# Performance work log

Measured on AMD Instinct MI355X. Metric: run time of the kernel, lower is better.

Reference implementation:

```python
import jax, jax.numpy as jnp
import numpy as np

T = 4096
EMBED = 1024
HEADS = 16


def setup_inputs() -> dict:
    key = jax.random.key(0)
    kx, kq, kk, kv = jax.random.split(key, 4)
    bound = 1.0 / np.sqrt(EMBED)
    x = jax.random.normal(kx, (T, EMBED), dtype=jnp.float32)
    Wq = jax.random.uniform(kq, (EMBED, EMBED), minval=-bound, maxval=bound, dtype=jnp.float32)
    Wk = jax.random.uniform(kk, (EMBED, EMBED), minval=-bound, maxval=bound, dtype=jnp.float32)
    Wv = jax.random.uniform(kv, (EMBED, EMBED), minval=-bound, maxval=bound, dtype=jnp.float32)
    return {"x": x, "Wq": Wq, "Wk": Wk, "Wv": Wv}


def reference(x, Wq, Wk, Wv):
    t, e = x.shape
    h = HEADS
    c = e // h  # head dim
    q = (x @ Wq).reshape(t, h, c)
    k = (x @ Wk).reshape(t, h, c)
    v = (x @ Wv).reshape(t, h, c)
    # scores: [h, t, t]
    scores = jnp.einsum('qhc,khc->hqk', q, k) / jnp.sqrt(jnp.asarray(c, x.dtype))
    causal = jnp.tril(jnp.ones((t, t), dtype=bool))
    scores = jnp.where(causal[None, :, :], scores, -jnp.inf)  # same as + log(tril)
    p = jax.nn.softmax(scores, axis=-1)
    y = jnp.einsum('hqk,khc->qhc', p, v)  # [t, h, c]
    return y.reshape(t, e)
```

## Files before the change

### kernel.cpp

```cpp
#include <hip/hip_runtime.h>
#include <hip/hip_bf16.h>

#define T_SEQ 4096
#define EMB 1024
#define NH 16
#define HD 64
#define QBLK 128
#define KVB 64
#define DEFER_THR 10.0f

typedef float f32x4 __attribute__((ext_vector_type(4)));
typedef float f32x16 __attribute__((ext_vector_type(16)));
typedef short short8 __attribute__((ext_vector_type(8)));
typedef short short4v __attribute__((ext_vector_type(4)));

__device__ inline unsigned short f2bf(float f) {
  union { float f; unsigned u; } a; a.f = f;
  unsigned r = a.u + 0x7fffu + ((a.u >> 16) & 1u);
  return (unsigned short)(r >> 16);
}
#if __has_builtin(__builtin_amdgcn_exp2f)
#define EXP2F(x) __builtin_amdgcn_exp2f(x)
#else
#define EXP2F(x) exp2f(x)
#endif
#define GLL16(g, l) __builtin_amdgcn_global_load_lds( \
    (const __attribute__((address_space(1))) void*)(g), \
    (__attribute__((address_space(3))) void*)(l), 16, 0, 0)

__global__ __launch_bounds__(256) void cast_x_kernel(const float* __restrict__ in,
                                                     unsigned short* __restrict__ out) {
  int i = (blockIdx.x * 256 + threadIdx.x) * 8;
  float4 a = *(const float4*)(in + i);
  float4 b = *(const float4*)(in + i + 4);
  uint4 o;
  o.x = f2bf(a.x) | ((unsigned)f2bf(a.y) << 16);
  o.y = f2bf(a.z) | ((unsigned)f2bf(a.w) << 16);
  o.z = f2bf(b.x) | ((unsigned)f2bf(b.y) << 16);
  o.w = f2bf(b.z) | ((unsigned)f2bf(b.w) << 16);
  *(uint4*)(out + i) = o;
}

__global__ __launch_bounds__(256) void transpose_cast_kernel(const float* __restrict__ Wq,
                                                             const float* __restrict__ Wk,
                                                             const float* __restrict__ Wv,
                                                             unsigned short* __restrict__ WTall) {
  int z = blockIdx.z;
  const float* W = (z == 0) ? Wq : ((z == 1) ? Wk : Wv);
  unsigned short* WT = WTall + (size_t)z * EMB * EMB;
  __shared__ unsigned short tile[32][33];
  int tx = threadIdx.x & 31, ty = threadIdx.x >> 5;
  int bn = blockIdx.x * 32, bk = blockIdx.y * 32;
#pragma unroll
  for (int p = 0; p < 4; p++)
    tile[ty + p * 8][tx] = f2bf(W[(size_t)(bk + ty + p * 8) * EMB + bn + tx]);
  __syncthreads();
#pragma unroll
  for (int p = 0; p < 4; p++)
    WT[(size_t)(bn + ty + p * 8) * EMB + bk + tx] = tile[tx][ty + p * 8];
}

__global__ __launch_bounds__(256) void gemm_qkv(const unsigned short* __restrict__ Xb,
                                                const unsigned short* __restrict__ WTall,
                                                unsigned short* __restrict__ QKV) {
  int z = blockIdx.z;
  const unsigned short* Bt = WTall + (size_t)z * EMB * EMB;
  unsigned short* Out = QKV + (size_t)z * T_SEQ * EMB;

  __shared__ __align__(16) unsigned short sA[128 * 32];
  __shared__ __align__(16) unsigned short sB[128 * 32];

  int m0 = blockIdx.x * 128, n0 = blockIdx.y * 128;
  int tid = threadIdx.x;
  int lane = tid & 63, wid = tid >> 6;
  int wr = wid >> 1, wc = wid & 1;
  int fr = lane & 15, fq = lane >> 4;

  int r0 = tid >> 2, o0 = (tid & 3) * 8;
  int r1 = (tid + 256) >> 2;

  f32x4 acc[4][4] = {};

  for (int k0 = 0; k0 < EMB; k0 += 32) {
    __syncthreads();
    GLL16(Xb + (size_t)(m0 + r0) * EMB + k0 + o0, sA + (size_t)tid * 8);
    GLL16(Xb + (size_t)(m0 + r1) * EMB + k0 + o0, sA + (size_t)(tid + 256) * 8);
    GLL16(Bt + (size_t)(n0 + r0) * EMB + k0 + o0, sB + (size_t)tid * 8);
    GLL16(Bt + (size_t)(n0 + r1) * EMB + k0 + o0, sB + (size_t)(tid + 256) * 8);
    asm volatile("s_waitcnt vmcnt(0)" ::: "memory");
    __syncthreads();

    short8 aF[4], bF[4];
#pragma unroll
    for (int i = 0; i < 4; i++) {
      aF[i] = *(const short8*)(sA + (wr * 64 + i * 16 + fr) * 32 + fq * 8);
      bF[i] = *(const short8*)(sB + (wc * 64 + i * 16 + fr) * 32 + fq * 8);
    }
#pragma unroll
    for (int i = 0; i < 4; i++)
#pragma unroll
      for (int j = 0; j < 4; j++)
        acc[i][j] = __builtin_amdgcn_mfma_f32_16x16x32_bf16(aF[i], bF[j], acc[i][j], 0, 0, 0);
  }

  if (z == 2) {
#pragma unroll
    for (int i = 0; i < 4; i++)
#pragma unroll
      for (int j = 0; j < 4; j++) {
        int col = n0 + wc * 64 + j * 16 + fr;
        int row0 = m0 + wr * 64 + i * 16 + fq * 4;
        short4v pk4;
#pragma unroll
        for (int r = 0; r < 4; r++) pk4[r] = (short)f2bf(acc[i][j][r]);
        *(short4v*)(Out + (size_t)col * T_SEQ + row0) = pk4;
      }
  } else {
    float scale = (z == 0) ? 0.1803368801111204f : 1.0f;
#pragma unroll
    for (int i = 0; i < 4; i++)
#pragma unroll
      for (int j = 0; j < 4; j++)
#pragma unroll
        for (int r = 0; r < 4; r++) {
          int row = m0 + wr * 64 + i * 16 + fq * 4 + r;
          int col = n0 + wc * 64 + j * 16 + fr;
          Out[(size_t)row * EMB + col] = f2bf(acc[i][j][r] * scale);
        }
  }
}

__global__ __launch_bounds__(256) void attn_kernel(const unsigned short* __restrict__ Qb,
                                                   const unsigned short* __restrict__ Kb,
                                                   const unsigned short* __restrict__ VTg,
                                                   float* __restrict__ out) {
  int qb = (gridDim.x - 1) - blockIdx.x;
  int h = blockIdx.y;
  int q0 = qb * QBLK;
  int tid = threadIdx.x;
  int lane = tid & 63, w = tid >> 6;
  int ql = lane & 31, hi = lane >> 5;

  __shared__ __align__(16) unsigned short smem[14336];
  unsigned short* sK = smem;
  unsigned short* sVT = smem + 64 * 72;
  unsigned short* sP = smem + 2 * 64 * 72 + w * (32 * 40);

  int wq0 = q0 + w * 32;
  int qg = wq0 + ql;

  short8 qf[4];
#pragma unroll
  for (int ks = 0; ks < 4; ks++)
    qf[ks] = *(const short8*)(Qb + (size_t)qg * EMB + h * HD + ks * 16 + hi * 8);

  f32x16 oT0 = {}, oT1 = {};
  float m = -1e30f, lsum = 0.f;

  int sr = tid >> 3;
  int scs = (tid & 7) * 8;

  int wqmax = wq0 + 31;
  int ntiles = (q0 + QBLK) / KVB;

  short8 ka = *(const short8*)(Kb + (size_t)(sr) * EMB + h * HD + scs);
  short8 kb = *(const short8*)(Kb + (size_t)(sr + 32) * EMB + h * HD + scs);
  short8 va = *(const short8*)(VTg + (size_t)(h * HD + sr) * T_SEQ + scs);
  short8 vb = *(const short8*)(VTg + (size_t)(h * HD + sr + 32) * T_SEQ + scs);

  for (int t = 0; t < ntiles; t++) {
    int kv0 = t * KVB;
    __syncthreads();
    *(short8*)(sK + sr * 72 + scs) = ka;
    *(short8*)(sK + (sr + 32) * 72 + scs) = kb;
    *(short8*)(sVT + sr * 72 + scs) = va;
    *(short8*)(sVT + (sr + 32) * 72 + scs) = vb;
    __syncthreads();

    if (t + 1 < ntiles) {
      int kv1 = kv0 + KVB;
      ka = *(const short8*)(Kb + (size_t)(kv1 + sr) * EMB + h * HD + scs);
      kb = *(const short8*)(Kb + (size_t)(kv1 + sr + 32) * EMB + h * HD + scs);
      va = *(const short8*)(VTg + (size_t)(h * HD + sr) * T_SEQ + kv1 + scs);
      vb = *(const short8*)(VTg + (size_t)(h * HD + sr + 32) * T_SEQ + kv1 + scs);
    }

#pragma unroll
    for (int s = 0; s < 2; s++) {
      int kvs = kv0 + s * 32;
      if (kvs <= wqmax) {
        f32x16 st = {};
        __builtin_amdgcn_s_setprio(1);
#pragma unroll
        for (int ks = 0; ks < 4; ks++) {
          short8 kf = *(const short8*)(sK + (s * 32 + ql) * 72 + ks * 16 + hi * 8);
          st = __builtin_amdgcn_mfma_f32_32x32x16_bf16(kf, qf[ks], st, 0, 0, 0);
        }
        __builtin_amdgcn_s_setprio(0);
        if (kvs + 31 > wq0) {
#pragma unroll
          for (int r = 0; r < 16; r++) {
            int kvg = kvs + (r & 3) + 8 * (r >> 2) + 4 * hi;
            if (kvg > qg) st[r] = -1e30f;
          }
        }
        float a0 = fmaxf(fmaxf(st[0], st[1]), st[2]);
        float a1 = fmaxf(fmaxf(st[3], st[4]), st[5]);
        float a2 = fmaxf(fmaxf(st[6], st[7]), st[8]);
        float a3 = fmaxf(fmaxf(st[9], st[10]), st[11]);
        float a4 = fmaxf(fmaxf(st[12], st[13]), st[14]);
        float mt = fmaxf(fmaxf(fmaxf(a0, a1), a2), fmaxf(fmaxf(a3, a4), st[15]));
        mt = fmaxf(mt, __shfl_xor(mt, 32));
        if (!__all(mt - m <= DEFER_THR)) {
          float mnew = fmaxf(m, mt);
          float al = EXP2F(m - mnew);
          lsum *= al;
#pragma unroll
          for (int r = 0; r < 16; r++) { oT0[r] *= al; oT1[r] *= al; }
          m = mnew;
        }
#pragma unroll
        for (int r = 0; r < 16; r++) st[r] = EXP2F(st[r] - m);
        float s0 = (st[0] + st[1]) + (st[2] + st[3]);
        float s1 = (st[4] + st[5]) + (st[6] + st[7]);
        float s2 = (st[8] + st[9]) + (st[10] + st[11]);
        float s3 = (st[12] + st[13]) + (st[14] + st[15]);
        float ls = (s0 + s1) + (s2 + s3);
        ls += __shfl_xor(ls, 32);
        lsum += ls;

#pragma unroll
        for (int g = 0; g < 4; g++) {
          __hip_bfloat162 plo = __float22bfloat162_rn(float2{st[g * 4 + 0], st[g * 4 + 1]});
          __hip_bfloat162 phi = __float22bfloat162_rn(float2{st[g * 4 + 2], st[g * 4 + 3]});
          union { __hip_bfloat162 h[2]; short4v s4; } u4;
          u4.h[0] = plo; u4.h[1] = phi;
          *(short4v*)(sP + ql * 40 + g * 8 + hi * 4) = u4.s4;
        }
        asm volatile("s_waitcnt lgkmcnt(0)" ::: "memory");
        __builtin_amdgcn_sched_barrier(0);

        __builtin_amdgcn_s_setprio(1);
#pragma unroll
        for (int ksp = 0; ksp < 2; ksp++) {
          short8 pa = *(const short8*)(sP + ql * 40 + ksp * 16 + hi * 8);
          int cb = s * 32 + ksp * 16 + hi * 8;
          short8 v0 = *(const short8*)(sVT + (0 * 32 + ql) * 72 + cb);
          short8 v1 = *(const short8*)(sVT + (1 * 32 + ql) * 72 + cb);
          oT0 = __builtin_amdgcn_mfma_f32_32x32x16_bf16(v0, pa, oT0, 0, 0, 0);
          oT1 = __builtin_amdgcn_mfma_f32_32x32x16_bf16(v1, pa, oT1, 0, 0, 0);
        }
        __builtin_amdgcn_s_setprio(0);
      }
    }
  }

  float inv = 1.0f / lsum;
  float* sw = (float*)smem + w * (32 * 36);
  int orow = lane >> 1, ocol = (lane & 1) * 16;
#pragma unroll
  for (int dt = 0; dt < 2; dt++) {
    __syncthreads();
#pragma unroll
    for (int r = 0; r < 16; r++) {
      int dl = (r & 3) + 8 * (r >> 2) + 4 * hi;
      sw[ql * 36 + dl] = (dt ? oT1[r] : oT0[r]) * inv;
    }
    __syncthreads();
#pragma unroll
    for (int c = 0; c < 4; c++) {
      f32x4 vv = *(const f32x4*)(sw + orow * 36 + ocol + c * 4);
      *(f32x4*)(out + (size_t)(wq0 + orow) * EMB + h * HD + dt * 32 + ocol + c * 4) = vv;
    }
  }
}

extern "C" void kernel_launch(void* const* d_in, const int* in_sizes, int n_in,
                              void* d_out, int out_size, void* d_ws, size_t ws_size,
                              hipStream_t stream) {
  const float* x  = (const float*)d_in[0];
  const float* Wq = (const float*)d_in[1];
  const float* Wk = (const float*)d_in[2];
  const float* Wv = (const float*)d_in[3];
  float* out = (float*)d_out;

  unsigned short* Qb = (unsigned short*)d_ws;
  unsigned short* Kb = Qb + (size_t)T_SEQ * EMB;
  unsigned short* VT = Kb + (size_t)T_SEQ * EMB;
  unsigned short* Xb = VT + (size_t)T_SEQ * EMB;
  unsigned short* WT = Xb + (size_t)T_SEQ * EMB;

  cast_x_kernel<<<(T_SEQ * EMB) / (256 * 8), 256, 0, stream>>>(x, Xb);
  dim3 tg(EMB / 32, EMB / 32, 3);
  transpose_cast_kernel<<<tg, 256, 0, stream>>>(Wq, Wk, Wv, WT);
  dim3 gg(T_SEQ / 128, EMB / 128, 3);
  gemm_qkv<<<gg, 256, 0, stream>>>(Xb, WT, Qb);
  dim3 ag(T_SEQ / QBLK, NH);
  attn_kernel<<<ag, 256, 0, stream>>>(Qb, Kb, VT, out);
}
```

Before: 251.0 us.

## Split KV range across waves per 32-query block with LDS merge of softmax partials

Attention now gives each block one 32-row query tile and spreads the causal KV sub-tiles round-robin across its four waves. K and V fragments are loaded straight from global memory into registers with no shared-memory staging or block barriers in the loop. Per-wave max and sum partials are then merged through LDS in a final reduction. V is written row-major by the GEMM and transposed by a separate new kernel, which adds a launch and extra traffic, and the launch-bounds hint now asks for more resident blocks.

```diff
diff --git a/kernel.cpp b/kernel.cpp
--- a/kernel.cpp
+++ b/kernel.cpp
@@ -5,8 +5,6 @@
 #define EMB 1024
 #define NH 16
 #define HD 64
-#define QBLK 128
-#define KVB 64
 #define DEFER_THR 10.0f
 
 typedef float f32x4 __attribute__((ext_vector_type(4)));
@@ -60,6 +58,21 @@
     WT[(size_t)(bn + ty + p * 8) * EMB + bk + tx] = tile[tx][ty + p * 8];
 }
 
+__global__ __launch_bounds__(256) void transpose_v_kernel(const unsigned short* __restrict__ V,
+                                                          unsigned short* __restrict__ VT) {
+  int h = blockIdx.z;
+  int t0 = blockIdx.x * 32, d0 = blockIdx.y * 32;
+  __shared__ unsigned short tl[32][33];
+  int tx = threadIdx.x & 31, ty = threadIdx.x >> 5;
+#pragma unroll
+  for (int p = 0; p < 4; p++)
+    tl[ty + p * 8][tx] = V[(size_t)(t0 + ty + p * 8) * EMB + h * HD + d0 + tx];
+  __syncthreads();
+#pragma unroll
+  for (int p = 0; p < 4; p++)
+    VT[(size_t)(h * HD + d0 + ty + p * 8) * T_SEQ + t0 + tx] = tl[tx][ty + p * 8];
+}
+
 __global__ __launch_bounds__(256) void gemm_qkv(const unsigned short* __restrict__ Xb,
                                                 const unsigned short* __restrict__ WTall,
                                                 unsigned short* __restrict__ QKV) {
@@ -103,51 +116,36 @@
         acc[i][j] = __builtin_amdgcn_mfma_f32_16x16x32_bf16(aF[i], bF[j], acc[i][j], 0, 0, 0);
   }
 
-  if (z == 2) {
-#pragma unroll
-    for (int i = 0; i < 4; i++)
-#pragma unroll
-      for (int j = 0; j < 4; j++) {
+  float scale = (z == 0) ? 0.1803368801111204f : 1.0f;
+#pragma unroll
+  for (int i = 0; i < 4; i++)
+#pragma unroll
+    for (int j = 0; j < 4; j++)
+#pragma unroll
+      for (int r = 0; r < 4; r++) {
+        int row = m0 + wr * 64 + i * 16 + fq * 4 + r;
         int col = n0 + wc * 64 + j * 16 + fr;
-        int row0 = m0 + wr * 64 + i * 16 + fq * 4;
-        short4v pk4;
-#pragma unroll
-        for (int r = 0; r < 4; r++) pk4[r] = (short)f2bf(acc[i][j][r]);
-        *(short4v*)(Out + (size_t)col * T_SEQ + row0) = pk4;
+        Out[(size_t)row * EMB + col] = f2bf(acc[i][j][r] * scale);
       }
-  } else {
-    float scale = (z == 0) ? 0.1803368801111204f : 1.0f;
-#pragma unroll
-    for (int i = 0; i < 4; i++)
-#pragma unroll
-      for (int j = 0; j < 4; j++)
-#pragma unroll
-        for (int r = 0; r < 4; r++) {
-          int row = m0 + wr * 64 + i * 16 + fq * 4 + r;
-          int col = n0 + wc * 64 + j * 16 + fr;
-          Out[(size_t)row * EMB + col] = f2bf(acc[i][j][r] * scale);
-        }
-  }
-}
-
-__global__ __launch_bounds__(256) void attn_kernel(const unsigned short* __restrict__ Qb,
-                                                   const unsigned short* __restrict__ Kb,
-                                                   const unsigned short* __restrict__ VTg,
-                                                   float* __restrict__ out) {
-  int qb = (gridDim.x - 1) - blockIdx.x;
+}
+
+__global__ __launch_bounds__(256, 4) void attn_kernel(const unsigned short* __restrict__ Qb,
+                                                      const unsigned short* __restrict__ Kb,
+                                                      const unsigned short* __restrict__ VTg,
+                                                      float* __restrict__ out) {
+  int c = (gridDim.x - 1) - blockIdx.x;
   int h = blockIdx.y;
-  int q0 = qb * QBLK;
   int tid = threadIdx.x;
   int lane = tid & 63, w = tid >> 6;
   int ql = lane & 31, hi = lane >> 5;
-
-  __shared__ __align__(16) unsigned short smem[14336];
-  unsigned short* sK = smem;
-  unsigned short* sVT = smem + 64 * 72;
-  unsigned short* sP = smem + 2 * 64 * 72 + w * (32 * 40);
-
-  int wq0 = q0 + w * 32;
-  int qg = wq0 + ql;
+  int wq0 = c * 32, qg = wq0 + ql;
+
+  __shared__ __align__(16) float smemf[4608];
+  unsigned short* sP = (unsigned short*)smemf + w * 1280;
+  float* bufA = smemf;
+  float* bufB = smemf + 2176;
+  float* sM = smemf + 4352;
+  float* sL = smemf + 4480;
 
   short8 qf[4];
 #pragma unroll
@@ -157,122 +155,117 @@
   f32x16 oT0 = {}, oT1 = {};
   float m = -1e30f, lsum = 0.f;
 
-  int sr = tid >> 3;
-  int scs = (tid & 7) * 8;
-
-  int wqmax = wq0 + 31;
-  int ntiles = (q0 + QBLK) / KVB;
-
-  short8 ka = *(const short8*)(Kb + (size_t)(sr) * EMB + h * HD + scs);
-  short8 kb = *(const short8*)(Kb + (size_t)(sr + 32) * EMB + h * HD + scs);
-  short8 va = *(const short8*)(VTg + (size_t)(h * HD + sr) * T_SEQ + scs);
-  short8 vb = *(const short8*)(VTg + (size_t)(h * HD + sr + 32) * T_SEQ + scs);
-
-  for (int t = 0; t < ntiles; t++) {
-    int kv0 = t * KVB;
-    __syncthreads();
-    *(short8*)(sK + sr * 72 + scs) = ka;
-    *(short8*)(sK + (sr + 32) * 72 + scs) = kb;
-    *(short8*)(sVT + sr * 72 + scs) = va;
-    *(short8*)(sVT + (sr + 32) * 72 + scs) = vb;
-    __syncthreads();
-
-    if (t + 1 < ntiles) {
-      int kv1 = kv0 + KVB;
-      ka = *(const short8*)(Kb + (size_t)(kv1 + sr) * EMB + h * HD + scs);
-      kb = *(const short8*)(Kb + (size_t)(kv1 + sr + 32) * EMB + h * HD + scs);
-      va = *(const short8*)(VTg + (size_t)(h * HD + sr) * T_SEQ + kv1 + scs);
-      vb = *(const short8*)(VTg + (size_t)(h * HD + sr + 32) * T_SEQ + kv1 + scs);
-    }
-
-#pragma unroll
-    for (int s = 0; s < 2; s++) {
-      int kvs = kv0 + s * 32;
-      if (kvs <= wqmax) {
-        f32x16 st = {};
-        __builtin_amdgcn_s_setprio(1);
-#pragma unroll
-        for (int ks = 0; ks < 4; ks++) {
-          short8 kf = *(const short8*)(sK + (s * 32 + ql) * 72 + ks * 16 + hi * 8);
-          st = __builtin_amdgcn_mfma_f32_32x32x16_bf16(kf, qf[ks], st, 0, 0, 0);
-        }
-        __builtin_amdgcn_s_setprio(0);
-        if (kvs + 31 > wq0) {
-#pragma unroll
-          for (int r = 0; r < 16; r++) {
-            int kvg = kvs + (r & 3) + 8 * (r >> 2) + 4 * hi;
-            if (kvg > qg) st[r] = -1e30f;
-          }
-        }
-        float a0 = fmaxf(fmaxf(st[0], st[1]), st[2]);
-        float a1 = fmaxf(fmaxf(st[3], st[4]), st[5]);
-        float a2 = fmaxf(fmaxf(st[6], st[7]), st[8]);
-        float a3 = fmaxf(fmaxf(st[9], st[10]), st[11]);
-        float a4 = fmaxf(fmaxf(st[12], st[13]), st[14]);
-        float mt = fmaxf(fmaxf(fmaxf(a0, a1), a2), fmaxf(fmaxf(a3, a4), st[15]));
-        mt = fmaxf(mt, __shfl_xor(mt, 32));
-        if (!__all(mt - m <= DEFER_THR)) {
-          float mnew = fmaxf(m, mt);
-          float al = EXP2F(m - mnew);
-          lsum *= al;
-#pragma unroll
-          for (int r = 0; r < 16; r++) { oT0[r] *= al; oT1[r] *= al; }
-          m = mnew;
-        }
-#pragma unroll
-        for (int r = 0; r < 16; r++) st[r] = EXP2F(st[r] - m);
-        float s0 = (st[0] + st[1]) + (st[2] + st[3]);
-        float s1 = (st[4] + st[5]) + (st[6] + st[7]);
-        float s2 = (st[8] + st[9]) + (st[10] + st[11]);
-        float s3 = (st[12] + st[13]) + (st[14] + st[15]);
-        float ls = (s0 + s1) + (s2 + s3);
-        ls += __shfl_xor(ls, 32);
-        lsum += ls;
-
-#pragma unroll
-        for (int g = 0; g < 4; g++) {
-          __hip_bfloat162 plo = __float22bfloat162_rn(float2{st[g * 4 + 0], st[g * 4 + 1]});
-          __hip_bfloat162 phi = __float22bfloat162_rn(float2{st[g * 4 + 2], st[g * 4 + 3]});
-          union { __hip_bfloat162 h[2]; short4v s4; } u4;
-          u4.h[0] = plo; u4.h[1] = phi;
-          *(short4v*)(sP + ql * 40 + g * 8 + hi * 4) = u4.s4;
-        }
-        asm volatile("s_waitcnt lgkmcnt(0)" ::: "memory");
-        __builtin_amdgcn_sched_barrier(0);
-
-        __builtin_amdgcn_s_setprio(1);
-#pragma unroll
-        for (int ksp = 0; ksp < 2; ksp++) {
-          short8 pa = *(const short8*)(sP + ql * 40 + ksp * 16 + hi * 8);
-          int cb = s * 32 + ksp * 16 + hi * 8;
-          short8 v0 = *(const short8*)(sVT + (0 * 32 + ql) * 72 + cb);
-          short8 v1 = *(const short8*)(sVT + (1 * 32 + ql) * 72 + cb);
-          oT0 = __builtin_amdgcn_mfma_f32_32x32x16_bf16(v0, pa, oT0, 0, 0, 0);
-          oT1 = __builtin_amdgcn_mfma_f32_32x32x16_bf16(v1, pa, oT1, 0, 0, 0);
-        }
-        __builtin_amdgcn_s_setprio(0);
+  for (int ss = w; ss <= c; ss += 4) {
+    int kvs = ss * 32;
+    const unsigned short* kbase = Kb + (size_t)(kvs + ql) * EMB + h * HD + hi * 8;
+    short8 kf0 = *(const short8*)(kbase);
+    short8 kf1 = *(const short8*)(kbase + 16);
+    short8 kf2 = *(const short8*)(kbase + 32);
+    short8 kf3 = *(const short8*)(kbase + 48);
+    const unsigned short* vbase = VTg + (size_t)(h * HD + ql) * T_SEQ + kvs + hi * 8;
+    short8 v00 = *(const short8*)(vbase);
+    short8 v01 = *(const short8*)(vbase + 16);
+    short8 v10 = *(const short8*)(vbase + 32 * T_SEQ);
+    short8 v11 = *(const short8*)(vbase + 32 * T_SEQ + 16);
+
+    f32x16 st = {};
+    __builtin_amdgcn_s_setprio(1);
+    st = __builtin_amdgcn_mfma_f32_32x32x16_bf16(kf0, qf[0], st, 0, 0, 0);
+    st = __builtin_amdgcn_mfma_f32_32x32x16_bf16(kf1, qf[1], st, 0, 0, 0);
+    st = __builtin_amdgcn_mfma_f32_32x32x16_bf16(kf2, qf[2], st, 0, 0, 0);
+    st = __builtin_amdgcn_mfma_f32_32x32x16_bf16(kf3, qf[3], st, 0, 0, 0);
+    __builtin_amdgcn_s_setprio(0);
+
+    if (ss == c) {
+#pragma unroll
+      for (int r = 0; r < 16; r++) {
+        int kvg = kvs + (r & 3) + 8 * (r >> 2) + 4 * hi;
+        if (kvg > qg) st[r] = -1e30f;
       }
     }
-  }
-
-  float inv = 1.0f / lsum;
-  float* sw = (float*)smem + w * (32 * 36);
-  int orow = lane >> 1, ocol = (lane & 1) * 16;
-#pragma unroll
-  for (int dt = 0; dt < 2; dt++) {
-    __syncthreads();
+    float a0 = fmaxf(fmaxf(st[0], st[1]), st[2]);
+    float a1 = fmaxf(fmaxf(st[3], st[4]), st[5]);
+    float a2 = fmaxf(fmaxf(st[6], st[7]), st[8]);
+    float a3 = fmaxf(fmaxf(st[9], st[10]), st[11]);
+    float a4 = fmaxf(fmaxf(st[12], st[13]), st[14]);
+    float mt = fmaxf(fmaxf(fmaxf(a0, a1), a2), fmaxf(fmaxf(a3, a4), st[15]));
+    mt = fmaxf(mt, __shfl_xor(mt, 32));
+    if (!__all(mt - m <= DEFER_THR)) {
+      float mnew = fmaxf(m, mt);
+      float al = EXP2F(m - mnew);
+      lsum *= al;
+#pragma unroll
+      for (int r = 0; r < 16; r++) { oT0[r] *= al; oT1[r] *= al; }
+      m = mnew;
+    }
+#pragma unroll
+    for (int r = 0; r < 16; r++) st[r] = EXP2F(st[r] - m);
+    float s0 = (st[0] + st[1]) + (st[2] + st[3]);
+    float s1 = (st[4] + st[5]) + (st[6] + st[7]);
+    float s2 = (st[8] + st[9]) + (st[10] + st[11]);
+    float s3 = (st[12] + st[13]) + (st[14] + st[15]);
+    float ls = (s0 + s1) + (s2 + s3);
+    ls += __shfl_xor(ls, 32);
+    lsum += ls;
+
+#pragma unroll
+    for (int g = 0; g < 4; g++) {
+      __hip_bfloat162 plo = __float22bfloat162_rn(float2{st[g * 4 + 0], st[g * 4 + 1]});
+      __hip_bfloat162 phi = __float22bfloat162_rn(float2{st[g * 4 + 2], st[g * 4 + 3]});
+      union { __hip_bfloat162 hh[2]; short4v s4; } u4;
+      u4.hh[0] = plo; u4.hh[1] = phi;
+      *(short4v*)(sP + ql * 40 + g * 8 + hi * 4) = u4.s4;
+    }
+    asm volatile("s_waitcnt lgkmcnt(0)" ::: "memory");
+    __builtin_amdgcn_sched_barrier(0);
+
+    short8 pa0 = *(const short8*)(sP + ql * 40 + hi * 8);
+    short8 pa1 = *(const short8*)(sP + ql * 40 + 16 + hi * 8);
+    __builtin_amdgcn_s_setprio(1);
+    oT0 = __builtin_amdgcn_mfma_f32_32x32x16_bf16(v00, pa0, oT0, 0, 0, 0);
+    oT1 = __builtin_amdgcn_mfma_f32_32x32x16_bf16(v10, pa0, oT1, 0, 0, 0);
+    oT0 = __builtin_amdgcn_mfma_f32_32x32x16_bf16(v01, pa1, oT0, 0, 0, 0);
+    oT1 = __builtin_amdgcn_mfma_f32_32x32x16_bf16(v11, pa1, oT1, 0, 0, 0);
+    __builtin_amdgcn_s_setprio(0);
+  }
+
+  if (hi == 0) { sM[w * 32 + ql] = m; sL[w * 32 + ql] = lsum; }
+  __syncthreads();
+  float m0 = sM[ql], m1 = sM[32 + ql], m2 = sM[64 + ql], m3 = sM[96 + ql];
+  float mF = fmaxf(fmaxf(m0, m1), fmaxf(m2, m3));
+  float lF = sL[ql] * EXP2F(m0 - mF) + sL[32 + ql] * EXP2F(m1 - mF) +
+             sL[64 + ql] * EXP2F(m2 - mF) + sL[96 + ql] * EXP2F(m3 - mF);
+  float fac = EXP2F(m - mF) / lF;
+
+  float* buf = (w < 2) ? bufA : bufB;
+  if ((w & 1) == 0) {
 #pragma unroll
     for (int r = 0; r < 16; r++) {
       int dl = (r & 3) + 8 * (r >> 2) + 4 * hi;
-      sw[ql * 36 + dl] = (dt ? oT1[r] : oT0[r]) * inv;
-    }
-    __syncthreads();
-#pragma unroll
-    for (int c = 0; c < 4; c++) {
-      f32x4 vv = *(const f32x4*)(sw + orow * 36 + ocol + c * 4);
-      *(f32x4*)(out + (size_t)(wq0 + orow) * EMB + h * HD + dt * 32 + ocol + c * 4) = vv;
-    }
-  }
+      buf[ql * 68 + dl] = oT0[r] * fac;
+      buf[ql * 68 + 32 + dl] = oT1[r] * fac;
+    }
+  }
+  __syncthreads();
+  if (w & 1) {
+#pragma unroll
+    for (int r = 0; r < 16; r++) {
+      int dl = (r & 3) + 8 * (r >> 2) + 4 * hi;
+      buf[ql * 68 + dl] += oT0[r] * fac;
+      buf[ql * 68 + 32 + dl] += oT1[r] * fac;
+    }
+  }
+  __syncthreads();
+  for (int i = tid; i < 2048; i += 256) {
+    int q = i >> 6, d = i & 63;
+    bufA[q * 68 + d] += bufB[q * 68 + d];
+  }
+  __syncthreads();
+  int q = tid >> 3, c8 = (tid & 7) * 8;
+  f32x4 va = *(const f32x4*)(bufA + q * 68 + c8);
+  f32x4 vb = *(const f32x4*)(bufA + q * 68 + c8 + 4);
+  *(f32x4*)(out + (size_t)(wq0 + q) * EMB + h * HD + c8) = va;
+  *(f32x4*)(out + (size_t)(wq0 + q) * EMB + h * HD + c8 + 4) = vb;
 }
 
 extern "C" void kernel_launch(void* const* d_in, const int* in_sizes, int n_in,
@@ -286,7 +279,8 @@
 
   unsigned short* Qb = (unsigned short*)d_ws;
   unsigned short* Kb = Qb + (size_t)T_SEQ * EMB;
-  unsigned short* VT = Kb + (size_t)T_SEQ * EMB;
+  unsigned short* Vb = Kb + (size_t)T_SEQ * EMB;
+  unsigned short* VT = Vb + (size_t)T_SEQ * EMB;
   unsigned short* Xb = VT + (size_t)T_SEQ * EMB;
   unsigned short* WT = Xb + (size_t)T_SEQ * EMB;
 
@@ -295,6 +289,8 @@
   transpose_cast_kernel<<<tg, 256, 0, stream>>>(Wq, Wk, Wv, WT);
   dim3 gg(T_SEQ / 128, EMB / 128, 3);
   gemm_qkv<<<gg, 256, 0, stream>>>(Xb, WT, Qb);
-  dim3 ag(T_SEQ / QBLK, NH);
+  dim3 tv(T_SEQ / 32, HD / 32, NH);
+  transpose_v_kernel<<<tv, 256, 0, stream>>>(Vb, VT);
+  dim3 ag(T_SEQ / 32, NH);
   attn_kernel<<<ag, 256, 0, stream>>>(Qb, Kb, VT, out);
 }
```

Result: slower. 285.2 us (+13.6%).

## Split causal attention KV range across two blocks and merge with combine kernel

Applied to the files above, without the earlier changes.

The attention grid gains a second z-dimension so each query block's KV tiles are split by parity between two workgroups. Each workgroup writes unnormalized partial outputs plus per-row max and sum, and a new combine kernel merges them. This aims to double parallelism and balance the causal workload across the GPU. The cost is extra fp32 partial-output traffic, two additional kernel launches, and a separate V transpose kernel that replaces the transposed store in the GEMM epilogue.

```diff
diff --git a/kernel.cpp b/kernel.cpp
--- a/kernel.cpp
+++ b/kernel.cpp
@@ -60,6 +60,21 @@
     WT[(size_t)(bn + ty + p * 8) * EMB + bk + tx] = tile[tx][ty + p * 8];
 }
 
+__global__ __launch_bounds__(256) void transpose_v_kernel(const unsigned short* __restrict__ V,
+                                                          unsigned short* __restrict__ VT) {
+  int h = blockIdx.z;
+  int t0 = blockIdx.x * 32, d0 = blockIdx.y * 32;
+  __shared__ unsigned short tl[32][33];
+  int tx = threadIdx.x & 31, ty = threadIdx.x >> 5;
+#pragma unroll
+  for (int p = 0; p < 4; p++)
+    tl[ty + p * 8][tx] = V[(size_t)(t0 + ty + p * 8) * EMB + h * HD + d0 + tx];
+  __syncthreads();
+#pragma unroll
+  for (int p = 0; p < 4; p++)
+    VT[(size_t)(h * HD + d0 + ty + p * 8) * T_SEQ + t0 + tx] = tl[tx][ty + p * 8];
+}
+
 __global__ __launch_bounds__(256) void gemm_qkv(const unsigned short* __restrict__ Xb,
                                                 const unsigned short* __restrict__ WTall,
                                                 unsigned short* __restrict__ QKV) {
@@ -103,40 +118,29 @@
         acc[i][j] = __builtin_amdgcn_mfma_f32_16x16x32_bf16(aF[i], bF[j], acc[i][j], 0, 0, 0);
   }
 
-  if (z == 2) {
-#pragma unroll
-    for (int i = 0; i < 4; i++)
-#pragma unroll
-      for (int j = 0; j < 4; j++) {
+  float scale = (z == 0) ? 0.1803368801111204f : 1.0f;
+#pragma unroll
+  for (int i = 0; i < 4; i++)
+#pragma unroll
+    for (int j = 0; j < 4; j++)
+#pragma unroll
+      for (int r = 0; r < 4; r++) {
+        int row = m0 + wr * 64 + i * 16 + fq * 4 + r;
         int col = n0 + wc * 64 + j * 16 + fr;
-        int row0 = m0 + wr * 64 + i * 16 + fq * 4;
-        short4v pk4;
-#pragma unroll
-        for (int r = 0; r < 4; r++) pk4[r] = (short)f2bf(acc[i][j][r]);
-        *(short4v*)(Out + (size_t)col * T_SEQ + row0) = pk4;
+        Out[(size_t)row * EMB + col] = f2bf(acc[i][j][r] * scale);
       }
-  } else {
-    float scale = (z == 0) ? 0.1803368801111204f : 1.0f;
-#pragma unroll
-    for (int i = 0; i < 4; i++)
-#pragma unroll
-      for (int j = 0; j < 4; j++)
-#pragma unroll
-        for (int r = 0; r < 4; r++) {
-          int row = m0 + wr * 64 + i * 16 + fq * 4 + r;
-          int col = n0 + wc * 64 + j * 16 + fr;
-          Out[(size_t)row * EMB + col] = f2bf(acc[i][j][r] * scale);
-        }
-  }
 }
 
 __global__ __launch_bounds__(256) void attn_kernel(const unsigned short* __restrict__ Qb,
                                                    const unsigned short* __restrict__ Kb,
                                                    const unsigned short* __restrict__ VTg,
-                                                   float* __restrict__ out) {
-  int qb = (gridDim.x - 1) - blockIdx.x;
+                                                   float* __restrict__ Opart,
+                                                   float* __restrict__ Mst,
+                                                   float* __restrict__ Lst) {
+  int c = (gridDim.x - 1) - blockIdx.x;
   int h = blockIdx.y;
-  int q0 = qb * QBLK;
+  int z = blockIdx.z;
+  int q0 = c * QBLK;
   int tid = threadIdx.x;
   int lane = tid & 63, w = tid >> 6;
   int ql = lane & 31, hi = lane >> 5;
@@ -161,101 +165,109 @@
   int scs = (tid & 7) * 8;
 
   int wqmax = wq0 + 31;
-  int ntiles = (q0 + QBLK) / KVB;
-
-  short8 ka = *(const short8*)(Kb + (size_t)(sr) * EMB + h * HD + scs);
-  short8 kb = *(const short8*)(Kb + (size_t)(sr + 32) * EMB + h * HD + scs);
-  short8 va = *(const short8*)(VTg + (size_t)(h * HD + sr) * T_SEQ + scs);
-  short8 vb = *(const short8*)(VTg + (size_t)(h * HD + sr + 32) * T_SEQ + scs);
-
-  for (int t = 0; t < ntiles; t++) {
-    int kv0 = t * KVB;
-    __syncthreads();
-    *(short8*)(sK + sr * 72 + scs) = ka;
-    *(short8*)(sK + (sr + 32) * 72 + scs) = kb;
-    *(short8*)(sVT + sr * 72 + scs) = va;
-    *(short8*)(sVT + (sr + 32) * 72 + scs) = vb;
-    __syncthreads();
-
-    if (t + 1 < ntiles) {
-      int kv1 = kv0 + KVB;
-      ka = *(const short8*)(Kb + (size_t)(kv1 + sr) * EMB + h * HD + scs);
-      kb = *(const short8*)(Kb + (size_t)(kv1 + sr + 32) * EMB + h * HD + scs);
-      va = *(const short8*)(VTg + (size_t)(h * HD + sr) * T_SEQ + kv1 + scs);
-      vb = *(const short8*)(VTg + (size_t)(h * HD + sr + 32) * T_SEQ + kv1 + scs);
-    }
-
-#pragma unroll
-    for (int s = 0; s < 2; s++) {
-      int kvs = kv0 + s * 32;
-      if (kvs <= wqmax) {
-        f32x16 st = {};
-        __builtin_amdgcn_s_setprio(1);
-#pragma unroll
-        for (int ks = 0; ks < 4; ks++) {
-          short8 kf = *(const short8*)(sK + (s * 32 + ql) * 72 + ks * 16 + hi * 8);
-          st = __builtin_amdgcn_mfma_f32_32x32x16_bf16(kf, qf[ks], st, 0, 0, 0);
+  int ntot = 2 * c + 2;
+
+  {
+    int kv0 = z * KVB;
+    short8 ka = *(const short8*)(Kb + (size_t)(kv0 + sr) * EMB + h * HD + scs);
+    short8 kb = *(const short8*)(Kb + (size_t)(kv0 + sr + 32) * EMB + h * HD + scs);
+    short8 va = *(const short8*)(VTg + (size_t)(h * HD + sr) * T_SEQ + kv0 + scs);
+    short8 vb = *(const short8*)(VTg + (size_t)(h * HD + sr + 32) * T_SEQ + kv0 + scs);
+
+    for (int t = z; t < ntot; t += 2) {
+      int kv0c = t * KVB;
+      __syncthreads();
+      *(short8*)(sK + sr * 72 + scs) = ka;
+      *(short8*)(sK + (sr + 32) * 72 + scs) = kb;
+      *(short8*)(sVT + sr * 72 + scs) = va;
+      *(short8*)(sVT + (sr + 32) * 72 + scs) = vb;
+      __syncthreads();
+
+      if (t + 2 < ntot) {
+        int kv1 = kv0c + 2 * KVB;
+        ka = *(const short8*)(Kb + (size_t)(kv1 + sr) * EMB + h * HD + scs);
+        kb = *(const short8*)(Kb + (size_t)(kv1 + sr + 32) * EMB + h * HD + scs);
+        va = *(const short8*)(VTg + (size_t)(h * HD + sr) * T_SEQ + kv1 + scs);
+        vb = *(const short8*)(VTg + (size_t)(h * HD + sr + 32) * T_SEQ + kv1 + scs);
+      }
+
+#pragma unroll
+      for (int s = 0; s < 2; s++) {
+        int kvs = kv0c + s * 32;
+        if (kvs <= wqmax) {
+          f32x16 st = {};
+          __builtin_amdgcn_s_setprio(1);
+#pragma unroll
+          for (int ks = 0; ks < 4; ks++) {
+            short8 kf = *(const short8*)(sK + (s * 32 + ql) * 72 + ks * 16 + hi * 8);
+            st = __builtin_amdgcn_mfma_f32_32x32x16_bf16(kf, qf[ks], st, 0, 0, 0);
+          }
+          __builtin_amdgcn_s_setprio(0);
+          if (kvs + 31 > wq0) {
+#pragma unroll
+            for (int r = 0; r < 16; r++) {
+              int kvg = kvs + (r & 3) + 8 * (r >> 2) + 4 * hi;
+              if (kvg > qg) st[r] = -1e30f;
+            }
+          }
+          float a0 = fmaxf(fmaxf(st[0], st[1]), st[2]);
+          float a1 = fmaxf(fmaxf(st[3], st[4]), st[5]);
+          float a2 = fmaxf(fmaxf(st[6], st[7]), st[8]);
+          float a3 = fmaxf(fmaxf(st[9], st[10]), st[11]);
+          float a4 = fmaxf(fmaxf(st[12], st[13]), st[14]);
+          float mt = fmaxf(fmaxf(fmaxf(a0, a1), a2), fmaxf(fmaxf(a3, a4), st[15]));
+          mt = fmaxf(mt, __shfl_xor(mt, 32));
+          if (!__all(mt - m <= DEFER_THR)) {
+            float mnew = fmaxf(m, mt);
+            float al = EXP2F(m - mnew);
+            lsum *= al;
+#pragma unroll
+            for (int r = 0; r < 16; r++) { oT0[r] *= al; oT1[r] *= al; }
+            m = mnew;
+          }
+#pragma unroll
+          for (int r = 0; r < 16; r++) st[r] = EXP2F(st[r] - m);
+          float s0 = (st[0] + st[1]) + (st[2] + st[3]);
+          float s1 = (st[4] + st[5]) + (st[6] + st[7]);
+          float s2 = (st[8] + st[9]) + (st[10] + st[11]);
+          float s3 = (st[12] + st[13]) + (st[14] + st[15]);
+          float ls = (s0 + s1) + (s2 + s3);
+          ls += __shfl_xor(ls, 32);
+          lsum += ls;
+
+#pragma unroll
+          for (int g = 0; g < 4; g++) {
+            __hip_bfloat162 plo = __float22bfloat162_rn(float2{st[g * 4 + 0], st[g * 4 + 1]});
+            __hip_bfloat162 phi = __float22bfloat162_rn(float2{st[g * 4 + 2], st[g * 4 + 3]});
+            union { __hip_bfloat162 hh[2]; short4v s4; } u4;
+            u4.hh[0] = plo; u4.hh[1] = phi;
+            *(short4v*)(sP + ql * 40 + g * 8 + hi * 4) = u4.s4;
+          }
+          asm volatile("s_waitcnt lgkmcnt(0)" ::: "memory");
+          __builtin_amdgcn_sched_barrier(0);
+
+          __builtin_amdgcn_s_setprio(1);
+#pragma unroll
+          for (int ksp = 0; ksp < 2; ksp++) {
+            short8 pa = *(const short8*)(sP + ql * 40 + ksp * 16 + hi * 8);
+            int cb = s * 32 + ksp * 16 + hi * 8;
+            short8 v0 = *(const short8*)(sVT + (0 * 32 + ql) * 72 + cb);
+            short8 v1 = *(const short8*)(sVT + (1 * 32 + ql) * 72 + cb);
+            oT0 = __builtin_amdgcn_mfma_f32_32x32x16_bf16(v0, pa, oT0, 0, 0, 0);
+            oT1 = __builtin_amdgcn_mfma_f32_32x32x16_bf16(v1, pa, oT1, 0, 0, 0);
+          }
+          __builtin_amdgcn_s_setprio(0);
         }
-        __builtin_amdgcn_s_setprio(0);
-        if (kvs + 31 > wq0) {
-#pragma unroll
-          for (int r = 0; r < 16; r++) {
-            int kvg = kvs + (r & 3) + 8 * (r >> 2) + 4 * hi;
-            if (kvg > qg) st[r] = -1e30f;
-          }
-        }
-        float a0 = fmaxf(fmaxf(st[0], st[1]), st[2]);
-        float a1 = fmaxf(fmaxf(st[3], st[4]), st[5]);
-        float a2 = fmaxf(fmaxf(st[6], st[7]), st[8]);
-        float a3 = fmaxf(fmaxf(st[9], st[10]), st[11]);
-        float a4 = fmaxf(fmaxf(st[12], st[13]), st[14]);
-        float mt = fmaxf(fmaxf(fmaxf(a0, a1), a2), fmaxf(fmaxf(a3, a4), st[15]));
-        mt = fmaxf(mt, __shfl_xor(mt, 32));
-        if (!__all(mt - m <= DEFER_THR)) {
-          float mnew = fmaxf(m, mt);
-          float al = EXP2F(m - mnew);
-          lsum *= al;
-#pragma unroll
-          for (int r = 0; r < 16; r++) { oT0[r] *= al; oT1[r] *= al; }
-          m = mnew;
-        }
-#pragma unroll
-        for (int r = 0; r < 16; r++) st[r] = EXP2F(st[r] - m);
-        float s0 = (st[0] + st[1]) + (st[2] + st[3]);
-        float s1 = (st[4] + st[5]) + (st[6] + st[7]);
-        float s2 = (st[8] + st[9]) + (st[10] + st[11]);
-        float s3 = (st[12] + st[13]) + (st[14] + st[15]);
-        float ls = (s0 + s1) + (s2 + s3);
-        ls += __shfl_xor(ls, 32);
-        lsum += ls;
-
-#pragma unroll
-        for (int g = 0; g < 4; g++) {
-          __hip_bfloat162 plo = __float22bfloat162_rn(float2{st[g * 4 + 0], st[g * 4 + 1]});
-          __hip_bfloat162 phi = __float22bfloat162_rn(float2{st[g * 4 + 2], st[g * 4 + 3]});
-          union { __hip_bfloat162 h[2]; short4v s4; } u4;
-          u4.h[0] = plo; u4.h[1] = phi;
-          *(short4v*)(sP + ql * 40 + g * 8 + hi * 4) = u4.s4;
-        }
-        asm volatile("s_waitcnt lgkmcnt(0)" ::: "memory");
-        __builtin_amdgcn_sched_barrier(0);
-
-        __builtin_amdgcn_s_setprio(1);
-#pragma unroll
-        for (int ksp = 0; ksp < 2; ksp++) {
-          short8 pa = *(const short8*)(sP + ql * 40 + ksp * 16 + hi * 8);
-          int cb = s * 32 + ksp * 16 + hi * 8;
-          short8 v0 = *(const short8*)(sVT + (0 * 32 + ql) * 72 + cb);
-          short8 v1 = *(const short8*)(sVT + (1 * 32 + ql) * 72 + cb);
-          oT0 = __builtin_amdgcn_mfma_f32_32x32x16_bf16(v0, pa, oT0, 0, 0, 0);
-          oT1 = __builtin_amdgcn_mfma_f32_32x32x16_bf16(v1, pa, oT1, 0, 0, 0);
-        }
-        __builtin_amdgcn_s_setprio(0);
       }
     }
   }
 
-  float inv = 1.0f / lsum;
+  if (hi == 0) {
+    Mst[((size_t)z * NH + h) * T_SEQ + qg] = m;
+    Lst[((size_t)z * NH + h) * T_SEQ + qg] = lsum;
+  }
+
+  float* Od = Opart + (size_t)z * T_SEQ * EMB;
   float* sw = (float*)smem + w * (32 * 36);
   int orow = lane >> 1, ocol = (lane & 1) * 16;
 #pragma unroll
@@ -264,15 +276,37 @@
 #pragma unroll
     for (int r = 0; r < 16; r++) {
       int dl = (r & 3) + 8 * (r >> 2) + 4 * hi;
-      sw[ql * 36 + dl] = (dt ? oT1[r] : oT0[r]) * inv;
+      sw[ql * 36 + dl] = dt ? oT1[r] : oT0[r];
     }
     __syncthreads();
 #pragma unroll
-    for (int c = 0; c < 4; c++) {
-      f32x4 vv = *(const f32x4*)(sw + orow * 36 + ocol + c * 4);
-      *(f32x4*)(out + (size_t)(wq0 + orow) * EMB + h * HD + dt * 32 + ocol + c * 4) = vv;
+    for (int cc = 0; cc < 4; cc++) {
+      f32x4 vv = *(const f32x4*)(sw + orow * 36 + ocol + cc * 4);
+      *(f32x4*)(Od + (size_t)(wq0 + orow) * EMB + h * HD + dt * 32 + ocol + cc * 4) = vv;
     }
   }
+}
+
+__global__ __launch_bounds__(256) void combine_kernel(const float* __restrict__ Opart,
+                                                      const float* __restrict__ Mst,
+                                                      const float* __restrict__ Lst,
+                                                      float* __restrict__ out) {
+  int i = (blockIdx.x * 256 + threadIdx.x) * 8;
+  int t = i >> 10, e = i & (EMB - 1), h = e >> 6;
+  float m0 = Mst[(size_t)h * T_SEQ + t], m1 = Mst[(size_t)(NH + h) * T_SEQ + t];
+  float l0 = Lst[(size_t)h * T_SEQ + t], l1 = Lst[(size_t)(NH + h) * T_SEQ + t];
+  float mF = fmaxf(m0, m1);
+  float w0 = EXP2F(m0 - mF), w1 = EXP2F(m1 - mF);
+  float inv = 1.0f / (l0 * w0 + l1 * w1);
+  w0 *= inv; w1 *= inv;
+  const float* O1 = Opart + (size_t)T_SEQ * EMB;
+  f32x4 a0 = *(const f32x4*)(Opart + i), a1 = *(const f32x4*)(Opart + i + 4);
+  f32x4 b0 = *(const f32x4*)(O1 + i),    b1 = *(const f32x4*)(O1 + i + 4);
+  f32x4 r0, r1;
+#pragma unroll
+  for (int j = 0; j < 4; j++) { r0[j] = a0[j] * w0 + b0[j] * w1; r1[j] = a1[j] * w0 + b1[j] * w1; }
+  *(f32x4*)(out + i) = r0;
+  *(f32x4*)(out + i + 4) = r1;
 }
 
 extern "C" void kernel_launch(void* const* d_in, const int* in_sizes, int n_in,
@@ -286,15 +320,22 @@
 
   unsigned short* Qb = (unsigned short*)d_ws;
   unsigned short* Kb = Qb + (size_t)T_SEQ * EMB;
-  unsigned short* VT = Kb + (size_t)T_SEQ * EMB;
+  unsigned short* Vb = Kb + (size_t)T_SEQ * EMB;
+  unsigned short* VT = Vb + (size_t)T_SEQ * EMB;
   unsigned short* Xb = VT + (size_t)T_SEQ * EMB;
   unsigned short* WT = Xb + (size_t)T_SEQ * EMB;
+  float* Opart = (float*)(WT + (size_t)3 * EMB * EMB);
+  float* Mst = Opart + (size_t)2 * T_SEQ * EMB;
+  float* Lst = Mst + (size_t)2 * NH * T_SEQ;
 
   cast_x_kernel<<<(T_SEQ * EMB) / (256 * 8), 256, 0, stream>>>(x, Xb);
   dim3 tg(EMB / 32, EMB / 32, 3);
   transpose_cast_kernel<<<tg, 256, 0, stream>>>(Wq, Wk, Wv, WT);
   dim3 gg(T_SEQ / 128, EMB / 128, 3);
   gemm_qkv<<<gg, 256, 0, stream>>>(Xb, WT, Qb);
-  dim3 ag(T_SEQ / QBLK, NH);
-  attn_kernel<<<ag, 256, 0, stream>>>(Qb, Kb, VT, out);
-}
+  dim3 tv(T_SEQ / 32, HD / 32, NH);
+  transpose_v_kernel<<<tv, 256, 0, stream>>>(Vb, VT);
+  dim3 ag(T_SEQ / QBLK, NH, 2);
+  attn_kernel<<<ag, 256, 0, stream>>>(Qb, Kb, VT, Opart, Mst, Lst);
+  combine_kernel<<<(T_SEQ * EMB) / (256 * 8), 256, 0, stream>>>(Opart, Mst, Lst, out);
+}
```

New measurement: 245.4 us. 1.02x faster.
